# Optimization experiments

Hardware: AMD Instinct MI355X
Metric: run time of the kernel (lower is better)

Reference implementation:

```python
import jax, jax.numpy as jnp
import numpy as np

NUM_HEADS = 6
WIN = 16
NW = 16   # number of windows sharing one mask (b_ % NW == 0)


def setup_inputs() -> dict:
    key = jax.random.key(0)
    ks = jax.random.split(key, 6)
    b_, n, dim = 256, WIN * WIN, 192
    qkv = jax.random.normal(ks[0], (b_, n, 3 * dim), dtype=jnp.float32)
    rpi = jax.random.randint(ks[1], (n, n), 0, (2 * WIN - 1) * (2 * WIN - 1))
    # additive attention mask per window-group (Swin uses 0 / -100; randn is fine for math)
    mask = jax.random.normal(ks[2], (NW, n, n), dtype=jnp.float32)
    rpb_table = 0.02 * jax.random.normal(ks[3], ((2 * WIN - 1) * (2 * WIN - 1), NUM_HEADS), dtype=jnp.float32)
    proj_w = jax.random.normal(ks[4], (dim, dim), dtype=jnp.float32) * (1.0 / np.sqrt(dim))
    proj_b = jax.random.normal(ks[5], (dim,), dtype=jnp.float32) * 0.01
    return {"qkv": qkv, "rpi": rpi, "mask": mask, "rpb_table": rpb_table,
            "proj_w": proj_w, "proj_b": proj_b}


def reference(qkv, rpi, mask, rpb_table, proj_w, proj_b):
    b_, n, c3 = qkv.shape
    c = c3 // 3
    h = NUM_HEADS
    hd = c // h
    scale = float(hd) ** -0.5
    # (b_, n, 3, h, hd) -> (3, b_, h, n, hd)
    qkv = qkv.reshape(b_, n, 3, h, hd).transpose(2, 0, 3, 1, 4)
    q, k, v = qkv[0] * scale, qkv[1], qkv[2]
    attn = jnp.einsum('bhqd,bhkd->bhqk', q, k)  # [b_, h, n, n]
    # gathered relative position bias: [n, n, h] -> [h, n, n]
    bias = rpb_table[rpi].transpose(2, 0, 1)
    attn = attn + bias[None]
    # add per-window-group mask: [b_//nw, nw, h, n, n]
    nw = mask.shape[0]
    attn = attn.reshape(b_ // nw, nw, h, n, n) + mask[None, :, None]
    attn = attn.reshape(b_, h, n, n)
    attn = jax.nn.softmax(attn, axis=-1)
    x = jnp.einsum('bhqk,bhkd->bhqd', attn, v)  # [b_, h, n, hd]
    x = x.transpose(0, 2, 1, 3).reshape(b_, n, c)
    # nn.Linear: x @ W^T + b
    return x @ proj_w.T + proj_b
```

## Files before the change

kernel.cpp:

```cpp
#include <hip/hip_runtime.h>
#include <hip/hip_bf16.h>

typedef _Float16 f16;
typedef _Float16 f16x2 __attribute__((ext_vector_type(2)));
typedef _Float16 f16x4 __attribute__((ext_vector_type(4)));
typedef _Float16 f16x8 __attribute__((ext_vector_type(8)));
typedef float f32x4 __attribute__((ext_vector_type(4)));

#define NHEADS 6
#define NTOK 256
#define NWINS 256
#define DIM 192
#define HD 32
#define C3 576
#define SCALE 0.17677669529663687f

__global__ __launch_bounds__(256) void prep_cb_kernel(const int* __restrict__ rpi,
                                                      const float* __restrict__ mask,
                                                      const float* __restrict__ rpb,
                                                      f16* __restrict__ cb) {
  int idx = blockIdx.x * 256 + threadIdx.x;
  int k = idx & 255;
  int q = (idx >> 8) & 255;
  int t = idx >> 16;
  int h = t % 6;
  int mg = t / 6;
  float v = rpb[rpi[(q << 8) | k] * 6 + h] + mask[(mg << 16) | (q << 8) | k];
  cb[idx] = (f16)v;
}

__global__ __launch_bounds__(256) void prep_w_kernel(const float* __restrict__ w,
                                                     f16* __restrict__ w16) {
  int i = blockIdx.x * 256 + threadIdx.x;
  if (i < DIM * DIM) w16[i] = (f16)w[i];
}

__global__ __launch_bounds__(256, 3) void attn_kernel(const float* __restrict__ qkv,
                                                      const f16* __restrict__ cb,
                                                      f16* __restrict__ x16) {
  const int idx = blockIdx.x;
  const int b = idx & 255;
  const int qh = (idx >> 8) & 1;
  const int h = idx >> 9;
  const int tid = threadIdx.x;
  const int lane = tid & 63;
  const int wave = tid >> 6;
  const int g = lane >> 4;
  const int r16 = lane & 15;

  __shared__ f16 Klin[16 * 64 * 8];
  __shared__ f16 VT[32][264];

  const int qbase = qh * 128 + wave * 32;
  const size_t cb_base = ((size_t)((b & 15) * 6 + h)) << 16;
  const f16* cbp0 = cb + cb_base + ((size_t)(qbase + r16) << 8) + g * 4;

  const int srow = tid >> 3;
  const int part = tid & 7;
  const float* kbase = qkv + (size_t)(b * NTOK + srow) * C3 + DIM + h * HD + part * 4;
  float4 ka[4], va[4], kb[4], vb[4];
#pragma unroll
  for (int rg = 0; rg < 4; ++rg) {
    const float* kp = kbase + (size_t)(rg * 32) * C3;
    ka[rg] = *(const float4*)kp;
    va[rg] = *(const float4*)(kp + DIM);
  }
#pragma unroll
  for (int rg = 0; rg < 4; ++rg) {
    const float* kp = kbase + (size_t)(rg * 32 + 128) * C3;
    kb[rg] = *(const float4*)kp;
    vb[rg] = *(const float4*)(kp + DIM);
  }

  f16x4 cv0[16];
#pragma unroll
  for (int i = 0; i < 16; ++i) cv0[i] = *((const f16x4*)(cbp0 + i * 16));

  const float* qp0 = qkv + (size_t)(b * NTOK + qbase + r16) * C3 + h * HD + g * 8;
  float4 qa0 = ((const float4*)qp0)[0];
  float4 qa1 = ((const float4*)qp0)[1];
  const float* qp1 = qp0 + 16 * C3;
  float4 qb0 = ((const float4*)qp1)[0];
  float4 qb1 = ((const float4*)qp1)[1];

  const int gg = part >> 1;
  const int half = part & 1;
#pragma unroll
  for (int rg = 0; rg < 4; ++rg) {
    const int row = rg * 32 + srow;
    const int slot = ((row >> 4) * 64) + gg * 16 + ((row & 15) ^ (gg << 2));
    f16x4 kf;
    kf[0] = (f16)ka[rg].x; kf[1] = (f16)ka[rg].y; kf[2] = (f16)ka[rg].z; kf[3] = (f16)ka[rg].w;
    *((f16x4*)&Klin[slot * 8 + half * 4]) = kf;
    const int d0 = part * 4;
    VT[d0 + 0][row ^ (((d0 + 0) & 7) << 2)] = (f16)va[rg].x;
    VT[d0 + 1][row ^ (((d0 + 1) & 7) << 2)] = (f16)va[rg].y;
    VT[d0 + 2][row ^ (((d0 + 2) & 7) << 2)] = (f16)va[rg].z;
    VT[d0 + 3][row ^ (((d0 + 3) & 7) << 2)] = (f16)va[rg].w;
  }
#pragma unroll
  for (int rg = 0; rg < 4; ++rg) {
    const int row = rg * 32 + srow + 128;
    const int slot = ((row >> 4) * 64) + gg * 16 + ((row & 15) ^ (gg << 2));
    f16x4 kf;
    kf[0] = (f16)kb[rg].x; kf[1] = (f16)kb[rg].y; kf[2] = (f16)kb[rg].z; kf[3] = (f16)kb[rg].w;
    *((f16x4*)&Klin[slot * 8 + half * 4]) = kf;
    const int d0 = part * 4;
    VT[d0 + 0][row ^ (((d0 + 0) & 7) << 2)] = (f16)vb[rg].x;
    VT[d0 + 1][row ^ (((d0 + 1) & 7) << 2)] = (f16)vb[rg].y;
    VT[d0 + 2][row ^ (((d0 + 2) & 7) << 2)] = (f16)vb[rg].z;
    VT[d0 + 3][row ^ (((d0 + 3) & 7) << 2)] = (f16)vb[rg].w;
  }

  f16x8 qfA, qfB;
  qfA[0] = (f16)(qa0.x * SCALE); qfA[1] = (f16)(qa0.y * SCALE);
  qfA[2] = (f16)(qa0.z * SCALE); qfA[3] = (f16)(qa0.w * SCALE);
  qfA[4] = (f16)(qa1.x * SCALE); qfA[5] = (f16)(qa1.y * SCALE);
  qfA[6] = (f16)(qa1.z * SCALE); qfA[7] = (f16)(qa1.w * SCALE);
  qfB[0] = (f16)(qb0.x * SCALE); qfB[1] = (f16)(qb0.y * SCALE);
  qfB[2] = (f16)(qb0.z * SCALE); qfB[3] = (f16)(qb0.w * SCALE);
  qfB[4] = (f16)(qb1.x * SCALE); qfB[5] = (f16)(qb1.y * SCALE);
  qfB[6] = (f16)(qb1.z * SCALE); qfB[7] = (f16)(qb1.w * SCALE);

  __syncthreads();

  const int krd = (lane & 48) + ((lane & 15) ^ ((lane >> 2) & 12));

  f16x4 cv1[16];

#pragma unroll
  for (int c = 0; c < 2; ++c) {
    const int qrow = qbase + c * 16 + r16;
    const f16x8 qf = (c == 0) ? qfA : qfB;

    f32x4 acc[16];
#pragma unroll
    for (int kt = 0; kt < 16; ++kt) {
      acc[kt][0] = 0.f; acc[kt][1] = 0.f; acc[kt][2] = 0.f; acc[kt][3] = 0.f;
    }
#pragma unroll
    for (int kt = 0; kt < 16; ++kt) {
      f16x8 af = *((const f16x8*)&Klin[(kt * 64 + krd) * 8]);
      acc[kt] = __builtin_amdgcn_mfma_f32_16x16x32_f16(af, qf, acc[kt], 0, 0, 0);
    }

    float m = -1e30f;
#pragma unroll
    for (int kt = 0; kt < 16; ++kt) {
      f16x4 cv = (c == 0) ? cv0[kt] : cv1[kt];
#pragma unroll
      for (int r = 0; r < 4; ++r) {
        acc[kt][r] += (float)cv[r];
        m = fmaxf(m, acc[kt][r]);
      }
    }

    if (c == 0) {
      const f16* cbp1 = cbp0 + 16 * 256;
#pragma unroll
      for (int i = 0; i < 16; ++i) cv1[i] = *((const f16x4*)(cbp1 + i * 16));
    }

    m = fmaxf(m, __shfl_xor(m, 16));
    m = fmaxf(m, __shfl_xor(m, 32));

    float s = 0.f;
#pragma unroll
    for (int kt = 0; kt < 16; ++kt) {
#pragma unroll
      for (int r = 0; r < 4; ++r) {
        float p = __expf(acc[kt][r] - m);
        acc[kt][r] = p;
        s += p;
      }
    }
    s += __shfl_xor(s, 16);
    s += __shfl_xor(s, 32);
    const float rinv = 1.0f / s;

    f32x4 xacc[2];
#pragma unroll
    for (int dt = 0; dt < 2; ++dt) {
      xacc[dt][0] = 0.f; xacc[dt][1] = 0.f; xacc[dt][2] = 0.f; xacc[dt][3] = 0.f;
    }
#pragma unroll
    for (int kt = 0; kt < 16; ++kt) {
      f16x4 pf;
      pf[0] = (f16)acc[kt][0]; pf[1] = (f16)acc[kt][1];
      pf[2] = (f16)acc[kt][2]; pf[3] = (f16)acc[kt][3];
#pragma unroll
      for (int dt = 0; dt < 2; ++dt) {
        const int vrow = dt * 16 + r16;
        const int col = (kt * 16 + g * 4) ^ ((r16 & 7) << 2);
        f16x4 vf = *((const f16x4*)&VT[vrow][col]);
        xacc[dt] = __builtin_amdgcn_mfma_f32_16x16x16f16(vf, pf, xacc[dt], 0, 0, 0);
      }
    }

    f16* xp = x16 + (size_t)(b * NTOK + qrow) * DIM + h * HD;
#pragma unroll
    for (int dt = 0; dt < 2; ++dt) {
      f16x4 xo;
      xo[0] = (f16)(xacc[dt][0] * rinv); xo[1] = (f16)(xacc[dt][1] * rinv);
      xo[2] = (f16)(xacc[dt][2] * rinv); xo[3] = (f16)(xacc[dt][3] * rinv);
      *((f16x4*)(xp + dt * 16 + g * 4)) = xo;
    }
  }
}

__global__ __launch_bounds__(256) void proj_kernel(const f16* __restrict__ x16,
                                                   const f16* __restrict__ w16,
                                                   const float* __restrict__ pb,
                                                   float* __restrict__ out) {
  const int lane = threadIdx.x & 63;
  const int wave = threadIdx.x >> 6;
  const int g = lane >> 4;
  const int r16 = lane & 15;
  const int m0 = blockIdx.x * 64 + wave * 16;

  f32x4 acc[12];
#pragma unroll
  for (int jt = 0; jt < 12; ++jt) {
    acc[jt][0] = 0.f; acc[jt][1] = 0.f; acc[jt][2] = 0.f; acc[jt][3] = 0.f;
  }
#pragma unroll
  for (int cc = 0; cc < 6; ++cc) {
    f16x8 af = *((const f16x8*)(x16 + (size_t)(m0 + r16) * DIM + cc * 32 + g * 8));
#pragma unroll
    for (int jt = 0; jt < 12; ++jt) {
      f16x8 bf = *((const f16x8*)(w16 + (size_t)(jt * 16 + r16) * DIM + cc * 32 + g * 8));
      acc[jt] = __builtin_amdgcn_mfma_f32_16x16x32_f16(af, bf, acc[jt], 0, 0, 0);
    }
  }
#pragma unroll
  for (int jt = 0; jt < 12; ++jt) {
    int j = jt * 16 + r16;
    float bias = pb[j];
#pragma unroll
    for (int r = 0; r < 4; ++r) {
      out[(size_t)(m0 + g * 4 + r) * DIM + j] = acc[jt][r] + bias;
    }
  }
}

extern "C" void kernel_launch(void* const* d_in, const int* in_sizes, int n_in,
                              void* d_out, int out_size, void* d_ws, size_t ws_size,
                              hipStream_t stream) {
  const float* qkv  = (const float*)d_in[0];
  const int*   rpi  = (const int*)d_in[1];
  const float* mask = (const float*)d_in[2];
  const float* rpb  = (const float*)d_in[3];
  const float* pw   = (const float*)d_in[4];
  const float* pbv  = (const float*)d_in[5];
  float* out = (float*)d_out;

  char* ws = (char*)d_ws;
  f16* cb  = (f16*)ws;
  f16* x16 = (f16*)(ws + 12582912);
  f16* w16 = (f16*)(ws + 12582912 + 25165824);

  prep_cb_kernel<<<24576, 256, 0, stream>>>(rpi, mask, rpb, cb);
  prep_w_kernel<<<144, 256, 0, stream>>>(pw, w16);
  attn_kernel<<<3072, 256, 0, stream>>>(qkv, cb, x16);
  proj_kernel<<<1024, 256, 0, stream>>>(x16, w16, pbv, out);
}
```

Baseline: 126.6 us.

## Process full window per block, fold log2e into scale, use packed fp16 conversions

Each attention block now covers all 256 query rows of a window/head, with each wave looping over four 16-row chunks. This halves the grid so K/V staging into shared memory is done once per window-head instead of twice. The softmax switches to exp2 by folding log2(e) into the Q scale and the precomputed bias, and uses split max/sum accumulators. fp32-to-fp16 casts use packed round-toward-zero conversions. The next chunk's bias and Q values are prefetched in the loop. Costs are fewer blocks in flight and slightly different rounding.

```diff
diff --git a/kernel.cpp b/kernel.cpp
--- a/kernel.cpp
+++ b/kernel.cpp
@@ -5,6 +5,7 @@
 typedef _Float16 f16x2 __attribute__((ext_vector_type(2)));
 typedef _Float16 f16x4 __attribute__((ext_vector_type(4)));
 typedef _Float16 f16x8 __attribute__((ext_vector_type(8)));
+typedef __fp16 h16x2 __attribute__((ext_vector_type(2)));
 typedef float f32x4 __attribute__((ext_vector_type(4)));
 
 #define NHEADS 6
@@ -13,7 +14,13 @@
 #define DIM 192
 #define HD 32
 #define C3 576
-#define SCALE 0.17677669529663687f
+#define LOG2E 1.4426950408889634f
+#define SCALE (0.17677669529663687f * LOG2E)
+
+__device__ inline f16x2 pkrtz(float a, float b) {
+  h16x2 r = __builtin_amdgcn_cvt_pkrtz(a, b);
+  return __builtin_bit_cast(f16x2, r);
+}
 
 __global__ __launch_bounds__(256) void prep_cb_kernel(const int* __restrict__ rpi,
                                                       const float* __restrict__ mask,
@@ -25,7 +32,7 @@
   int t = idx >> 16;
   int h = t % 6;
   int mg = t / 6;
-  float v = rpb[rpi[(q << 8) | k] * 6 + h] + mask[(mg << 16) | (q << 8) | k];
+  float v = (rpb[rpi[(q << 8) | k] * 6 + h] + mask[(mg << 16) | (q << 8) | k]) * LOG2E;
   cb[idx] = (f16)v;
 }
 
@@ -33,6 +40,16 @@
                                                      f16* __restrict__ w16) {
   int i = blockIdx.x * 256 + threadIdx.x;
   if (i < DIM * DIM) w16[i] = (f16)w[i];
+}
+
+__device__ inline f16x8 q_to_f16(float4 a, float4 b) {
+  f16x2 p0 = pkrtz(a.x * SCALE, a.y * SCALE);
+  f16x2 p1 = pkrtz(a.z * SCALE, a.w * SCALE);
+  f16x2 p2 = pkrtz(b.x * SCALE, b.y * SCALE);
+  f16x2 p3 = pkrtz(b.z * SCALE, b.w * SCALE);
+  f16x4 lo = __builtin_shufflevector(p0, p1, 0, 1, 2, 3);
+  f16x4 hi = __builtin_shufflevector(p2, p3, 0, 1, 2, 3);
+  return __builtin_shufflevector(lo, hi, 0, 1, 2, 3, 4, 5, 6, 7);
 }
 
 __global__ __launch_bounds__(256, 3) void attn_kernel(const float* __restrict__ qkv,
@@ -40,8 +57,7 @@
                                                       f16* __restrict__ x16) {
   const int idx = blockIdx.x;
   const int b = idx & 255;
-  const int qh = (idx >> 8) & 1;
-  const int h = idx >> 9;
+  const int h = idx >> 8;
   const int tid = threadIdx.x;
   const int lane = tid & 63;
   const int wave = tid >> 6;
@@ -51,9 +67,9 @@
   __shared__ f16 Klin[16 * 64 * 8];
   __shared__ f16 VT[32][264];
 
-  const int qbase = qh * 128 + wave * 32;
+  const int qbase = wave * 64;
   const size_t cb_base = ((size_t)((b & 15) * 6 + h)) << 16;
-  const f16* cbp0 = cb + cb_base + ((size_t)(qbase + r16) << 8) + g * 4;
+  const f16* cbp = cb + cb_base + ((size_t)(qbase + r16) << 8) + g * 4;
 
   const int srow = tid >> 3;
   const int part = tid & 7;
@@ -72,27 +88,24 @@
     vb[rg] = *(const float4*)(kp + DIM);
   }
 
-  f16x4 cv0[16];
-#pragma unroll
-  for (int i = 0; i < 16; ++i) cv0[i] = *((const f16x4*)(cbp0 + i * 16));
-
-  const float* qp0 = qkv + (size_t)(b * NTOK + qbase + r16) * C3 + h * HD + g * 8;
-  float4 qa0 = ((const float4*)qp0)[0];
-  float4 qa1 = ((const float4*)qp0)[1];
-  const float* qp1 = qp0 + 16 * C3;
-  float4 qb0 = ((const float4*)qp1)[0];
-  float4 qb1 = ((const float4*)qp1)[1];
+  f16x4 cv[16];
+#pragma unroll
+  for (int i = 0; i < 16; ++i) cv[i] = *((const f16x4*)(cbp + i * 16));
+
+  const float* qp = qkv + (size_t)(b * NTOK + qbase + r16) * C3 + h * HD + g * 8;
+  float4 qn0 = ((const float4*)qp)[0];
+  float4 qn1 = ((const float4*)qp)[1];
 
   const int gg = part >> 1;
   const int half = part & 1;
+  const int d0 = part * 4;
 #pragma unroll
   for (int rg = 0; rg < 4; ++rg) {
     const int row = rg * 32 + srow;
     const int slot = ((row >> 4) * 64) + gg * 16 + ((row & 15) ^ (gg << 2));
-    f16x4 kf;
-    kf[0] = (f16)ka[rg].x; kf[1] = (f16)ka[rg].y; kf[2] = (f16)ka[rg].z; kf[3] = (f16)ka[rg].w;
-    *((f16x4*)&Klin[slot * 8 + half * 4]) = kf;
-    const int d0 = part * 4;
+    f16x2 k01 = pkrtz(ka[rg].x, ka[rg].y);
+    f16x2 k23 = pkrtz(ka[rg].z, ka[rg].w);
+    *((f16x4*)&Klin[slot * 8 + half * 4]) = __builtin_shufflevector(k01, k23, 0, 1, 2, 3);
     VT[d0 + 0][row ^ (((d0 + 0) & 7) << 2)] = (f16)va[rg].x;
     VT[d0 + 1][row ^ (((d0 + 1) & 7) << 2)] = (f16)va[rg].y;
     VT[d0 + 2][row ^ (((d0 + 2) & 7) << 2)] = (f16)va[rg].z;
@@ -102,37 +115,23 @@
   for (int rg = 0; rg < 4; ++rg) {
     const int row = rg * 32 + srow + 128;
     const int slot = ((row >> 4) * 64) + gg * 16 + ((row & 15) ^ (gg << 2));
-    f16x4 kf;
-    kf[0] = (f16)kb[rg].x; kf[1] = (f16)kb[rg].y; kf[2] = (f16)kb[rg].z; kf[3] = (f16)kb[rg].w;
-    *((f16x4*)&Klin[slot * 8 + half * 4]) = kf;
-    const int d0 = part * 4;
+    f16x2 k01 = pkrtz(kb[rg].x, kb[rg].y);
+    f16x2 k23 = pkrtz(kb[rg].z, kb[rg].w);
+    *((f16x4*)&Klin[slot * 8 + half * 4]) = __builtin_shufflevector(k01, k23, 0, 1, 2, 3);
     VT[d0 + 0][row ^ (((d0 + 0) & 7) << 2)] = (f16)vb[rg].x;
     VT[d0 + 1][row ^ (((d0 + 1) & 7) << 2)] = (f16)vb[rg].y;
     VT[d0 + 2][row ^ (((d0 + 2) & 7) << 2)] = (f16)vb[rg].z;
     VT[d0 + 3][row ^ (((d0 + 3) & 7) << 2)] = (f16)vb[rg].w;
   }
 
-  f16x8 qfA, qfB;
-  qfA[0] = (f16)(qa0.x * SCALE); qfA[1] = (f16)(qa0.y * SCALE);
-  qfA[2] = (f16)(qa0.z * SCALE); qfA[3] = (f16)(qa0.w * SCALE);
-  qfA[4] = (f16)(qa1.x * SCALE); qfA[5] = (f16)(qa1.y * SCALE);
-  qfA[6] = (f16)(qa1.z * SCALE); qfA[7] = (f16)(qa1.w * SCALE);
-  qfB[0] = (f16)(qb0.x * SCALE); qfB[1] = (f16)(qb0.y * SCALE);
-  qfB[2] = (f16)(qb0.z * SCALE); qfB[3] = (f16)(qb0.w * SCALE);
-  qfB[4] = (f16)(qb1.x * SCALE); qfB[5] = (f16)(qb1.y * SCALE);
-  qfB[6] = (f16)(qb1.z * SCALE); qfB[7] = (f16)(qb1.w * SCALE);
+  f16x8 qf = q_to_f16(qn0, qn1);
 
   __syncthreads();
 
   const int krd = (lane & 48) + ((lane & 15) ^ ((lane >> 2) & 12));
 
-  f16x4 cv1[16];
-
-#pragma unroll
-  for (int c = 0; c < 2; ++c) {
-    const int qrow = qbase + c * 16 + r16;
-    const f16x8 qf = (c == 0) ? qfA : qfB;
-
+#pragma unroll
+  for (int c = 0; c < 4; ++c) {
     f32x4 acc[16];
 #pragma unroll
     for (int kt = 0; kt < 16; ++kt) {
@@ -144,36 +143,43 @@
       acc[kt] = __builtin_amdgcn_mfma_f32_16x16x32_f16(af, qf, acc[kt], 0, 0, 0);
     }
 
-    float m = -1e30f;
-#pragma unroll
-    for (int kt = 0; kt < 16; ++kt) {
-      f16x4 cv = (c == 0) ? cv0[kt] : cv1[kt];
-#pragma unroll
-      for (int r = 0; r < 4; ++r) {
-        acc[kt][r] += (float)cv[r];
-        m = fmaxf(m, acc[kt][r]);
-      }
-    }
-
-    if (c == 0) {
-      const f16* cbp1 = cbp0 + 16 * 256;
-#pragma unroll
-      for (int i = 0; i < 16; ++i) cv1[i] = *((const f16x4*)(cbp1 + i * 16));
-    }
-
+    float m0 = -1e30f, m1 = -1e30f, m2 = -1e30f, m3 = -1e30f;
+#pragma unroll
+    for (int kt = 0; kt < 16; ++kt) {
+      acc[kt][0] += (float)cv[kt][0];
+      acc[kt][1] += (float)cv[kt][1];
+      acc[kt][2] += (float)cv[kt][2];
+      acc[kt][3] += (float)cv[kt][3];
+      m0 = fmaxf(m0, acc[kt][0]);
+      m1 = fmaxf(m1, acc[kt][1]);
+      m2 = fmaxf(m2, acc[kt][2]);
+      m3 = fmaxf(m3, acc[kt][3]);
+    }
+
+    if (c < 3) {
+      const f16* cbn = cbp + (c + 1) * 4096;
+#pragma unroll
+      for (int i = 0; i < 16; ++i) cv[i] = *((const f16x4*)(cbn + i * 16));
+      const float* qpn = qp + (size_t)((c + 1) * 16) * C3;
+      qn0 = ((const float4*)qpn)[0];
+      qn1 = ((const float4*)qpn)[1];
+    }
+
+    float m = fmaxf(fmaxf(m0, m1), fmaxf(m2, m3));
     m = fmaxf(m, __shfl_xor(m, 16));
     m = fmaxf(m, __shfl_xor(m, 32));
 
-    float s = 0.f;
-#pragma unroll
-    for (int kt = 0; kt < 16; ++kt) {
-#pragma unroll
-      for (int r = 0; r < 4; ++r) {
-        float p = __expf(acc[kt][r] - m);
-        acc[kt][r] = p;
-        s += p;
-      }
-    }
+    float s0 = 0.f, s1 = 0.f, s2 = 0.f, s3 = 0.f;
+#pragma unroll
+    for (int kt = 0; kt < 16; ++kt) {
+      float p0 = __builtin_amdgcn_exp2f(acc[kt][0] - m);
+      float p1 = __builtin_amdgcn_exp2f(acc[kt][1] - m);
+      float p2 = __builtin_amdgcn_exp2f(acc[kt][2] - m);
+      float p3 = __builtin_amdgcn_exp2f(acc[kt][3] - m);
+      acc[kt][0] = p0; acc[kt][1] = p1; acc[kt][2] = p2; acc[kt][3] = p3;
+      s0 += p0; s1 += p1; s2 += p2; s3 += p3;
+    }
+    float s = (s0 + s1) + (s2 + s3);
     s += __shfl_xor(s, 16);
     s += __shfl_xor(s, 32);
     const float rinv = 1.0f / s;
@@ -185,9 +191,9 @@
     }
 #pragma unroll
     for (int kt = 0; kt < 16; ++kt) {
-      f16x4 pf;
-      pf[0] = (f16)acc[kt][0]; pf[1] = (f16)acc[kt][1];
-      pf[2] = (f16)acc[kt][2]; pf[3] = (f16)acc[kt][3];
+      f16x2 p01 = pkrtz(acc[kt][0], acc[kt][1]);
+      f16x2 p23 = pkrtz(acc[kt][2], acc[kt][3]);
+      f16x4 pf = __builtin_shufflevector(p01, p23, 0, 1, 2, 3);
 #pragma unroll
       for (int dt = 0; dt < 2; ++dt) {
         const int vrow = dt * 16 + r16;
@@ -197,14 +203,15 @@
       }
     }
 
-    f16* xp = x16 + (size_t)(b * NTOK + qrow) * DIM + h * HD;
+    f16* xp = x16 + (size_t)(b * NTOK + qbase + c * 16 + r16) * DIM + h * HD;
 #pragma unroll
     for (int dt = 0; dt < 2; ++dt) {
-      f16x4 xo;
-      xo[0] = (f16)(xacc[dt][0] * rinv); xo[1] = (f16)(xacc[dt][1] * rinv);
-      xo[2] = (f16)(xacc[dt][2] * rinv); xo[3] = (f16)(xacc[dt][3] * rinv);
-      *((f16x4*)(xp + dt * 16 + g * 4)) = xo;
-    }
+      f16x2 o01 = pkrtz(xacc[dt][0] * rinv, xacc[dt][1] * rinv);
+      f16x2 o23 = pkrtz(xacc[dt][2] * rinv, xacc[dt][3] * rinv);
+      *((f16x4*)(xp + dt * 16 + g * 4)) = __builtin_shufflevector(o01, o23, 0, 1, 2, 3);
+    }
+
+    if (c < 3) qf = q_to_f16(qn0, qn1);
   }
 }
 
@@ -261,6 +268,6 @@
 
   prep_cb_kernel<<<24576, 256, 0, stream>>>(rpi, mask, rpb, cb);
   prep_w_kernel<<<144, 256, 0, stream>>>(pw, w16);
-  attn_kernel<<<3072, 256, 0, stream>>>(qkv, cb, x16);
+  attn_kernel<<<1536, 256, 0, stream>>>(qkv, cb, x16);
   proj_kernel<<<1024, 256, 0, stream>>>(x16, w16, pbv, out);
 }
```

After: 122.3 us. 3.4% less time.
